# Performance work log

Measured on AMD Instinct MI355X. Metric: run time of the kernel, lower is better.

Reference implementation:

```python
import jax, jax.numpy as jnp
import numpy as np

B, L, H, F, E = 32, 512, 768, 3072, 8  # sentences, seq_len, hidden, ffn, experts


def setup_inputs() -> dict:
    key = jax.random.key(0)
    kx, kl, k1, k2, k3, k4 = jax.random.split(key, 6)
    return {
        "hidden_states": jax.random.normal(kx, (B, L, H), dtype=jnp.float32),
        "router_labels": jax.random.randint(kl, (B,), 0, E, dtype=jnp.int32),
        "W1": jax.random.normal(k1, (E, H, F), dtype=jnp.float32) * 0.02,
        "b1": jnp.zeros((E, F), dtype=jnp.float32),
        "W2": jax.random.normal(k2, (E, F, H), dtype=jnp.float32) * 0.02,
        "b2": jnp.zeros((E, H), dtype=jnp.float32),
    }


def reference(hidden_states, router_labels, W1, b1, W2, b2):
    # Equivalent to: sort sentences by label, run each group through its
    # expert FFN, concat, unsort. Expressed as a gather of per-sentence
    # expert weights followed by batched GEMMs (same math, no data-dependent
    # shapes).
    W1g = W1[router_labels]            # [B, H, F]
    b1g = b1[router_labels][:, None]   # [B, 1, F]
    W2g = W2[router_labels]            # [B, F, H]
    b2g = b2[router_labels][:, None]   # [B, 1, H]
    h = jnp.einsum("blh,bhf->blf", hidden_states, W1g) + b1g
    h = jax.nn.gelu(h, approximate=False)
    out = jnp.einsum("blf,bfh->blh", h, W2g) + b2g
    return out
```

## Files before the change

kernel.cpp:

```cpp
#include <hip/hip_runtime.h>
#include <hip/hip_bf16.h>

#define NB   32
#define SEQ  512
#define HID  768
#define FFN  3072
#define NEXP 8

typedef float f32x4 __attribute__((ext_vector_type(4)));
typedef short s16x8 __attribute__((ext_vector_type(8)));

__device__ __forceinline__ unsigned short f2bf(float f) {
    return __builtin_bit_cast(unsigned short, (__bf16)f);
}

__device__ __forceinline__ float fast_exp2(float x) {
    float r; asm("v_exp_f32 %0, %1" : "=v"(r) : "v"(x)); return r;
}
__device__ __forceinline__ float fast_rcp(float x) {
    float r; asm("v_rcp_f32 %0, %1" : "=v"(r) : "v"(x)); return r;
}

__device__ __forceinline__ float gelu_fast(float v) {
    float u  = v * (0.7978845608f + 0.0356774081f * v * v);
    float t  = fast_exp2(-2.8853900817779268f * fabsf(u));
    float T  = (1.0f - t) * fast_rcp(1.0f + t);
    return 0.5f * v + 0.5f * fabsf(v) * T;
}

#define GLOAD16(gp, lp) __builtin_amdgcn_global_load_lds( \
    (const __attribute__((address_space(1))) unsigned int*)(gp), \
    (__attribute__((address_space(3))) unsigned int*)(lp), 16, 0, 0)

#define VMCNT(N) asm volatile("s_waitcnt vmcnt(%0)" :: "i"(N) : "memory")

__global__ void sort_labels_kernel(const int* __restrict__ labels, int* __restrict__ perm)
{
    int i = threadIdx.x;
    if (i < NB) {
        int li = labels[i];
        int rank = 0;
        for (int j = 0; j < NB; j++) {
            int lj = labels[j];
            if (lj < li || (lj == li && j < i)) rank++;
        }
        perm[rank] = i;
    }
}

__global__ __launch_bounds__(256) void cvt_x_xcd(
    const float* __restrict__ X, const int* __restrict__ perm,
    unsigned short* __restrict__ Xb)
{
    const int L = blockIdx.x;
    const int xcd = L & 7, j = L >> 3;
    const int sent = perm[xcd * 4 + (j >> 3)];
    const int slab = j & 7;
    const size_t base = (size_t)sent * (SEQ * HID) + (size_t)slab * (SEQ * HID / 8);
    const float* src = X + base;
    unsigned short* dst = Xb + base;
    for (int i = threadIdx.x; i < SEQ * HID / 8 / 8; i += 256) {
        f32x4 a = *(const f32x4*)(src + (size_t)i * 8);
        f32x4 b = *(const f32x4*)(src + (size_t)i * 8 + 4);
        unsigned short o[8];
#pragma unroll
        for (int v = 0; v < 4; v++) o[v] = f2bf(a[v]);
#pragma unroll
        for (int v = 0; v < 4; v++) o[4 + v] = f2bf(b[v]);
        *(s16x8*)(dst + (size_t)i * 8) = *(s16x8*)o;
    }
}

__global__ __launch_bounds__(256) void cvt_transpose_kernel(
    const float* __restrict__ W, unsigned short* __restrict__ WT, int R, int C)
{
    __shared__ unsigned short tile[64][65];
    const int cb = blockIdx.x * 64, rb = blockIdx.y * 64;
    const float* src = W + (size_t)blockIdx.z * R * C;
    unsigned short* dst = WT + (size_t)blockIdx.z * R * C;
    const int x = threadIdx.x & 63, y0 = threadIdx.x >> 6;
#pragma unroll
    for (int i = 0; i < 16; i++) {
        int r = y0 + i * 4;
        tile[r][x] = f2bf(src[(size_t)(rb + r) * C + cb + x]);
    }
    __syncthreads();
#pragma unroll
    for (int i = 0; i < 16; i++) {
        int c = y0 + i * 4;
        dst[(size_t)(cb + c) * R + rb + x] = tile[x][c];
    }
}

template<int LDB, bool ISA>
__device__ __forceinline__ void stage_region(const char* g, char* lds, int half, int tid)
{
#pragma unroll
    for (int p = 0; p < 2; p++) {
        int L  = p * 8192 + tid * 16;
        int rr = L >> 7;
        int cb = L & 127;
        int row = ISA ? ((rr & 63) + ((rr >> 6) << 7) + half * 64)
                      : ((rr & 31) + ((rr >> 5) << 6) + half * 32);
        int cbs = cb ^ ((row & 7) << 4);
        GLOAD16(g + (size_t)row * LDB + cbs, lds + (size_t)row * 128 + cb);
    }
}

__device__ __forceinline__ void read_af(const char* Ab, int arow_b, int k0, int ih, s16x8 (&a)[2][4])
{
    const int k1 = k0 ^ 64;
#pragma unroll
    for (int i = 0; i < 4; i++) {
        const char* p = Ab + arow_b + (ih * 64 + i * 16) * 128;
        a[0][i] = *(const s16x8*)(p + k0);
        a[1][i] = *(const s16x8*)(p + k1);
    }
}
__device__ __forceinline__ void read_bf(const char* Bb, int brow_b, int k0, int jh, s16x8 (&b)[2][2])
{
    const int k1 = k0 ^ 64;
#pragma unroll
    for (int j = 0; j < 2; j++) {
        const char* p = Bb + brow_b + (jh * 32 + j * 16) * 128;
        b[0][j] = *(const s16x8*)(p + k0);
        b[1][j] = *(const s16x8*)(p + k1);
    }
}

template<int IH, int JH>
__device__ __forceinline__ void mfma_quad(s16x8 (&a)[2][4], s16x8 (&b)[2][2], f32x4 (&acc)[8][4])
{
    __builtin_amdgcn_s_setprio(1);
#pragma unroll
    for (int kk = 0; kk < 2; kk++)
#pragma unroll
        for (int i = 0; i < 4; i++)
#pragma unroll
            for (int j = 0; j < 2; j++)
                acc[IH * 4 + i][JH * 2 + j] = __builtin_amdgcn_mfma_f32_16x16x32_bf16(
                    a[kk][i], b[kk][j], acc[IH * 4 + i][JH * 2 + j], 0, 0, 0);
    __builtin_amdgcn_s_setprio(0);
}

template<int LDB, bool S1, bool S2, int VM>
__device__ __forceinline__ void gwindow(const char* AgK, const char* BgK,
    char* Acur, char* Bcur, char* Anxt, char* Bnxt,
    int arow_b, int brow_b, int k0, int tid, f32x4 (&acc)[8][4])
{
    s16x8 a[2][4], b0[2][2], b1[2][2];
    read_af(Acur, arow_b, k0, 0, a);
    read_bf(Bcur, brow_b, k0, 0, b0);
    if constexpr (S1) stage_region<LDB, true >(AgK + 128, Anxt, 1, tid);
    __builtin_amdgcn_s_barrier();
    mfma_quad<0, 0>(a, b0, acc);
    __builtin_amdgcn_s_barrier();
    read_bf(Bcur, brow_b, k0, 1, b1);
    if constexpr (S1) stage_region<LDB, false>(BgK + 128, Bnxt, 1, tid);
    __builtin_amdgcn_s_barrier();
    mfma_quad<0, 1>(a, b1, acc);
    __builtin_amdgcn_s_barrier();
    read_af(Acur, arow_b, k0, 1, a);
    if constexpr (S2) stage_region<LDB, true >(AgK + 256, Acur, 0, tid);
    __builtin_amdgcn_s_barrier();
    mfma_quad<1, 1>(a, b1, acc);
    __builtin_amdgcn_s_barrier();
    if constexpr (S2) stage_region<LDB, false>(BgK + 256, Bcur, 0, tid);
    __builtin_amdgcn_s_barrier();
    mfma_quad<1, 0>(a, b0, acc);
    if constexpr (VM >= 0) VMCNT(VM);
    __builtin_amdgcn_s_barrier();
}

template<int LDB>
__device__ __forceinline__ void gemm_mainloop(const char* Ag, const char* Bg,
    char* smem, int KT, int tid, int arow_b, int brow_b, int k0, f32x4 (&acc)[8][4])
{
    stage_region<LDB, true >(Ag,       smem,          0, tid);
    stage_region<LDB, false>(Bg,       smem + 65536,  0, tid);
    stage_region<LDB, true >(Ag,       smem,          1, tid);
    stage_region<LDB, false>(Bg,       smem + 65536,  1, tid);
    stage_region<LDB, true >(Ag + 128, smem + 32768,  0, tid);
    stage_region<LDB, false>(Bg + 128, smem + 98304,  0, tid);
    VMCNT(4);
    __builtin_amdgcn_s_barrier();

    int cur = 0;
    for (int kt = 0; kt < KT - 2; ++kt) {
        char* Acur = smem + (cur << 15);
        char* Anxt = smem + ((cur ^ 1) << 15);
        char* Bcur = smem + 65536 + (cur << 15);
        char* Bnxt = smem + 65536 + ((cur ^ 1) << 15);
        gwindow<LDB, true, true, 4>(Ag + (size_t)kt * 128, Bg + (size_t)kt * 128,
            Acur, Bcur, Anxt, Bnxt, arow_b, brow_b, k0, tid, acc);
        cur ^= 1;
    }
    {
        char* Acur = smem + (cur << 15);
        char* Anxt = smem + ((cur ^ 1) << 15);
        char* Bcur = smem + 65536 + (cur << 15);
        char* Bnxt = smem + 65536 + ((cur ^ 1) << 15);
        gwindow<LDB, true, false, 0>(Ag + (size_t)(KT - 2) * 128, Bg + (size_t)(KT - 2) * 128,
            Acur, Bcur, Anxt, Bnxt, arow_b, brow_b, k0, tid, acc);
        cur ^= 1;
    }
    {
        char* Acur = smem + (cur << 15);
        char* Anxt = smem + ((cur ^ 1) << 15);
        char* Bcur = smem + 65536 + (cur << 15);
        char* Bnxt = smem + 65536 + ((cur ^ 1) << 15);
        gwindow<LDB, false, false, -1>(Ag + (size_t)(KT - 1) * 128, Bg + (size_t)(KT - 1) * 128,
            Acur, Bcur, Anxt, Bnxt, arow_b, brow_b, k0, tid, acc);
    }
}

__global__ __launch_bounds__(512, 2) void moe_gemm1(
    const unsigned short* __restrict__ Xb,
    const int*   __restrict__ labels,
    const int*   __restrict__ perm,
    const unsigned short* __restrict__ W1T,
    const float* __restrict__ B1,
    unsigned short* __restrict__ G)
{
    extern __shared__ char smem[];
    const int L = blockIdx.x;
    const int xcd  = L & 7;
    const int r    = L >> 8;
    const int i    = (L >> 3) & 31;
    const int pair = i >> 2;
    const int bs = perm[xcd * 4 + (pair >> 1)];
    const int mt = pair & 1;
    const int nt = r * 4 + (i & 3);
    const int e  = labels[bs];

    const char* Ag = (const char*)(Xb + ((size_t)bs * SEQ + (size_t)mt * 256) * HID);
    const char* Bg = (const char*)(W1T + (size_t)e * FFN * HID + (size_t)nt * 256 * HID);

    const int tid = threadIdx.x;
    const int lane = tid & 63, w = tid >> 6;
    const int wm = (w >> 2) * 128, wn = (w & 3) * 64;
    const int fr = lane & 15, fq = lane >> 4;
    const int arow_b = (wm + fr) * 128, brow_b = (wn + fr) * 128;
    const int k0 = (fq * 16) ^ ((fr & 7) << 4);

    f32x4 acc[8][4];
#pragma unroll
    for (int i2 = 0; i2 < 8; i2++)
#pragma unroll
        for (int j = 0; j < 4; j++) acc[i2][j] = (f32x4)0.0f;

    gemm_mainloop<HID * 2>(Ag, Bg, smem, HID / 64, tid, arow_b, brow_b, k0, acc);

    const float* b1g = B1 + (size_t)e * FFN + (size_t)nt * 256;
    float bias[4];
#pragma unroll
    for (int nj = 0; nj < 4; nj++) bias[nj] = b1g[wn + nj * 16 + fr];
#pragma unroll
    for (int mi = 0; mi < 8; mi++)
#pragma unroll
        for (int nj = 0; nj < 4; nj++) {
            const int col = wn + nj * 16 + fr;
#pragma unroll
            for (int r2 = 0; r2 < 4; r2++) {
                const int row = wm + mi * 16 + fq * 4 + r2;
                float v = acc[mi][nj][r2] + bias[nj];
                int byte = row * 512 + ((col * 2) ^ ((row & 7) << 4));
                *(unsigned short*)(smem + byte) = f2bf(gelu_fast(v));
            }
        }
    __syncthreads();
    char* Cgb = (char*)(G + ((size_t)bs * SEQ + (size_t)mt * 256) * FFN + (size_t)nt * 256);
#pragma unroll
    for (int it = 0; it < 16; it++) {
        int chunk = tid + it * 512;
        int row = chunk >> 5;
        int cb  = (chunk & 31) * 16;
        s16x8 v = *(const s16x8*)(smem + row * 512 + (cb ^ ((row & 7) << 4)));
        __builtin_nontemporal_store(v, (s16x8*)(Cgb + (size_t)row * (FFN * 2) + cb));
    }
}

__global__ __launch_bounds__(512, 2) void moe_gemm2(
    const unsigned short* __restrict__ G,
    const int*   __restrict__ labels,
    const int*   __restrict__ perm,
    const unsigned short* __restrict__ W2T,
    const float* __restrict__ B2,
    float* __restrict__ Out)
{
    extern __shared__ char smem[];
    const int L = blockIdx.x;
    const int xcd = L & 7, s = L >> 3;
    const int bs = perm[xcd * 4 + s / 6];
    const int rr = s % 6;
    const int mt = rr / 3, nt = rr % 3;
    const int e  = labels[bs];

    const char* Ag = (const char*)(G + ((size_t)bs * SEQ + (size_t)mt * 256) * FFN);
    const char* Bg = (const char*)(W2T + (size_t)e * HID * FFN + (size_t)nt * 256 * FFN);

    const int tid = threadIdx.x;
    const int lane = tid & 63, w = tid >> 6;
    const int wm = (w >> 2) * 128, wn = (w & 3) * 64;
    const int fr = lane & 15, fq = lane >> 4;
    const int arow_b = (wm + fr) * 128, brow_b = (wn + fr) * 128;
    const int k0 = (fq * 16) ^ ((fr & 7) << 4);

    f32x4 acc[8][4];
#pragma unroll
    for (int i = 0; i < 8; i++)
#pragma unroll
        for (int j = 0; j < 4; j++) acc[i][j] = (f32x4)0.0f;

    gemm_mainloop<FFN * 2>(Ag, Bg, smem, FFN / 64, tid, arow_b, brow_b, k0, acc);

    const float* b2g = B2 + (size_t)e * HID + (size_t)nt * 256;
    float bias[4];
#pragma unroll
    for (int nj = 0; nj < 4; nj++) bias[nj] = b2g[wn + nj * 16 + fr];
    char* Cgb = (char*)(Out + ((size_t)bs * SEQ + (size_t)mt * 256) * HID + (size_t)nt * 256);

#pragma unroll
    for (int half = 0; half < 2; ++half) {
        if ((wn >> 7) == half) {
#pragma unroll
            for (int mi = 0; mi < 8; mi++)
#pragma unroll
                for (int nj = 0; nj < 4; nj++) {
                    const int lcol = (wn & 127) + nj * 16 + fr;
#pragma unroll
                    for (int r2 = 0; r2 < 4; r2++) {
                        const int row = wm + mi * 16 + fq * 4 + r2;
                        int byte = row * 512 + ((lcol * 4) ^ ((row & 7) << 4));
                        *(float*)(smem + byte) = acc[mi][nj][r2] + bias[nj];
                    }
                }
        }
        __syncthreads();
#pragma unroll
        for (int it = 0; it < 16; it++) {
            int chunk = tid + it * 512;
            int row = chunk >> 5;
            int cb  = (chunk & 31) * 16;
            f32x4 v = *(const f32x4*)(smem + row * 512 + (cb ^ ((row & 7) << 4)));
            __builtin_nontemporal_store(v, (f32x4*)(Cgb + (size_t)row * (HID * 4) + half * 512 + cb));
        }
        if (half == 0) __syncthreads();
    }
}

extern "C" void kernel_launch(void* const* d_in, const int* in_sizes, int n_in,
                              void* d_out, int out_size, void* d_ws, size_t ws_size,
                              hipStream_t stream) {
    const float* X      = (const float*)d_in[0];
    const int*   labels = (const int*)  d_in[1];
    const float* W1     = (const float*)d_in[2];
    const float* B1     = (const float*)d_in[3];
    const float* W2     = (const float*)d_in[4];
    const float* B2     = (const float*)d_in[5];
    float* Out = (float*)d_out;

    char* ws = (char*)d_ws;
    unsigned short* Xb  = (unsigned short*)(ws);
    unsigned short* W1T = (unsigned short*)(ws + 25165824);
    unsigned short* W2T = (unsigned short*)(ws + 62914560);
    unsigned short* G   = (unsigned short*)(ws + 100663296);
    int*            perm = (int*)(ws + 201326592);

    (void)hipFuncSetAttribute((const void*)moe_gemm1,
        hipFuncAttributeMaxDynamicSharedMemorySize, 131072);
    (void)hipFuncSetAttribute((const void*)moe_gemm2,
        hipFuncAttributeMaxDynamicSharedMemorySize, 131072);

    sort_labels_kernel<<<1, 64, 0, stream>>>(labels, perm);
    cvt_x_xcd<<<256, 256, 0, stream>>>(X, perm, Xb);
    cvt_transpose_kernel<<<dim3(FFN / 64, HID / 64, NEXP), 256, 0, stream>>>(W1, W1T, HID, FFN);
    cvt_transpose_kernel<<<dim3(HID / 64, FFN / 64, NEXP), 256, 0, stream>>>(W2, W2T, FFN, HID);

    moe_gemm1<<<768, dim3(512), 131072, stream>>>(Xb, labels, perm, W1T, B1, G);
    moe_gemm2<<<192, dim3(512), 131072, stream>>>(G, labels, perm, W2T, B2, Out);
}
```

Before: 243.7 us.

## Make GEMM1 blocks loop over three N tiles and simplify X conversion

GEMM1 now launches 256 blocks instead of 768. Each block computes three consecutive 256-wide FFN column tiles in sequence, reusing the same A rows and writing out the bias+GELU results for each tile. The X fp32-to-bf16 conversion becomes a plain grid-stride kernel that no longer orders its work by the sorted-sentence/XCD mapping. With 256 blocks at 2 per CU the grid is a single wave, which avoids tail effects but gives less scheduling slack. The A tile may also lose its warm-L2 placement from the old XCD-ordered conversion.

Measured after the change: 345.2 us. +41.7%, slower.

```diff
diff --git a/kernel.cpp b/kernel.cpp
--- a/kernel.cpp
+++ b/kernel.cpp
@@ -48,26 +48,20 @@
     }
 }
 
-__global__ __launch_bounds__(256) void cvt_x_xcd(
-    const float* __restrict__ X, const int* __restrict__ perm,
-    unsigned short* __restrict__ Xb)
-{
-    const int L = blockIdx.x;
-    const int xcd = L & 7, j = L >> 3;
-    const int sent = perm[xcd * 4 + (j >> 3)];
-    const int slab = j & 7;
-    const size_t base = (size_t)sent * (SEQ * HID) + (size_t)slab * (SEQ * HID / 8);
-    const float* src = X + base;
-    unsigned short* dst = Xb + base;
-    for (int i = threadIdx.x; i < SEQ * HID / 8 / 8; i += 256) {
-        f32x4 a = *(const f32x4*)(src + (size_t)i * 8);
-        f32x4 b = *(const f32x4*)(src + (size_t)i * 8 + 4);
+__global__ __launch_bounds__(256) void cvt_x_kernel(
+    const float* __restrict__ X, unsigned short* __restrict__ Xb, int n8)
+{
+    int idx = blockIdx.x * blockDim.x + threadIdx.x;
+    int stride = gridDim.x * blockDim.x;
+    for (int i = idx; i < n8; i += stride) {
+        f32x4 a = *(const f32x4*)(X + (size_t)i * 8);
+        f32x4 b = *(const f32x4*)(X + (size_t)i * 8 + 4);
         unsigned short o[8];
 #pragma unroll
         for (int v = 0; v < 4; v++) o[v] = f2bf(a[v]);
 #pragma unroll
         for (int v = 0; v < 4; v++) o[4 + v] = f2bf(b[v]);
-        *(s16x8*)(dst + (size_t)i * 8) = *(s16x8*)o;
+        *(s16x8*)(Xb + (size_t)i * 8) = *(s16x8*)o;
     }
 }
 
@@ -225,16 +219,14 @@
     extern __shared__ char smem[];
     const int L = blockIdx.x;
     const int xcd  = L & 7;
-    const int r    = L >> 8;
-    const int i    = (L >> 3) & 31;
-    const int pair = i >> 2;
-    const int bs = perm[xcd * 4 + (pair >> 1)];
-    const int mt = pair & 1;
-    const int nt = r * 4 + (i & 3);
-    const int e  = labels[bs];
+    const int slot = L >> 3;
+    const int pair = slot >> 2;
+    const int bs  = perm[xcd * 4 + (pair >> 1)];
+    const int mt  = pair & 1;
+    const int ntg = slot & 3;
+    const int e   = labels[bs];
 
     const char* Ag = (const char*)(Xb + ((size_t)bs * SEQ + (size_t)mt * 256) * HID);
-    const char* Bg = (const char*)(W1T + (size_t)e * FFN * HID + (size_t)nt * 256 * HID);
 
     const int tid = threadIdx.x;
     const int lane = tid & 63, w = tid >> 6;
@@ -243,40 +235,46 @@
     const int arow_b = (wm + fr) * 128, brow_b = (wn + fr) * 128;
     const int k0 = (fq * 16) ^ ((fr & 7) << 4);
 
-    f32x4 acc[8][4];
-#pragma unroll
-    for (int i2 = 0; i2 < 8; i2++)
-#pragma unroll
-        for (int j = 0; j < 4; j++) acc[i2][j] = (f32x4)0.0f;
-
-    gemm_mainloop<HID * 2>(Ag, Bg, smem, HID / 64, tid, arow_b, brow_b, k0, acc);
-
-    const float* b1g = B1 + (size_t)e * FFN + (size_t)nt * 256;
-    float bias[4];
-#pragma unroll
-    for (int nj = 0; nj < 4; nj++) bias[nj] = b1g[wn + nj * 16 + fr];
-#pragma unroll
-    for (int mi = 0; mi < 8; mi++)
-#pragma unroll
-        for (int nj = 0; nj < 4; nj++) {
-            const int col = wn + nj * 16 + fr;
-#pragma unroll
-            for (int r2 = 0; r2 < 4; r2++) {
-                const int row = wm + mi * 16 + fq * 4 + r2;
-                float v = acc[mi][nj][r2] + bias[nj];
-                int byte = row * 512 + ((col * 2) ^ ((row & 7) << 4));
-                *(unsigned short*)(smem + byte) = f2bf(gelu_fast(v));
+    for (int chunk = 0; chunk < 3; ++chunk) {
+        const int nt = ntg * 3 + chunk;
+        const char* Bg = (const char*)(W1T + (size_t)e * FFN * HID + (size_t)nt * 256 * HID);
+
+        f32x4 acc[8][4];
+#pragma unroll
+        for (int i2 = 0; i2 < 8; i2++)
+#pragma unroll
+            for (int j = 0; j < 4; j++) acc[i2][j] = (f32x4)0.0f;
+
+        gemm_mainloop<HID * 2>(Ag, Bg, smem, HID / 64, tid, arow_b, brow_b, k0, acc);
+
+        const float* b1g = B1 + (size_t)e * FFN + (size_t)nt * 256;
+        float bias[4];
+#pragma unroll
+        for (int nj = 0; nj < 4; nj++) bias[nj] = b1g[wn + nj * 16 + fr];
+#pragma unroll
+        for (int mi = 0; mi < 8; mi++)
+#pragma unroll
+            for (int nj = 0; nj < 4; nj++) {
+                const int col = wn + nj * 16 + fr;
+#pragma unroll
+                for (int r2 = 0; r2 < 4; r2++) {
+                    const int row = wm + mi * 16 + fq * 4 + r2;
+                    float v = acc[mi][nj][r2] + bias[nj];
+                    int byte = row * 512 + ((col * 2) ^ ((row & 7) << 4));
+                    *(unsigned short*)(smem + byte) = f2bf(gelu_fast(v));
+                }
             }
+        __syncthreads();
+        char* Cgb = (char*)(G + ((size_t)bs * SEQ + (size_t)mt * 256) * FFN + (size_t)nt * 256);
+#pragma unroll
+        for (int it = 0; it < 16; it++) {
+            int c2 = tid + it * 512;
+            int row = c2 >> 5;
+            int cb  = (c2 & 31) * 16;
+            s16x8 v = *(const s16x8*)(smem + row * 512 + (cb ^ ((row & 7) << 4)));
+            __builtin_nontemporal_store(v, (s16x8*)(Cgb + (size_t)row * (FFN * 2) + cb));
         }
-    __syncthreads();
-    char* Cgb = (char*)(G + ((size_t)bs * SEQ + (size_t)mt * 256) * FFN + (size_t)nt * 256);
-#pragma unroll
-    for (int it = 0; it < 16; it++) {
-        int chunk = tid + it * 512;
-        int row = chunk >> 5;
-        int cb  = (chunk & 31) * 16;
-        s16x8 v = *(const s16x8*)(smem + row * 512 + (cb ^ ((row & 7) << 4)));
-        __builtin_nontemporal_store(v, (s16x8*)(Cgb + (size_t)row * (FFN * 2) + cb));
+        __syncthreads();
     }
 }
 
@@ -373,10 +371,10 @@
         hipFuncAttributeMaxDynamicSharedMemorySize, 131072);
 
     sort_labels_kernel<<<1, 64, 0, stream>>>(labels, perm);
-    cvt_x_xcd<<<256, 256, 0, stream>>>(X, perm, Xb);
+    cvt_x_kernel<<<2048, 256, 0, stream>>>(X, Xb, NB * SEQ * HID / 8);
     cvt_transpose_kernel<<<dim3(FFN / 64, HID / 64, NEXP), 256, 0, stream>>>(W1, W1T, HID, FFN);
     cvt_transpose_kernel<<<dim3(HID / 64, FFN / 64, NEXP), 256, 0, stream>>>(W2, W2T, FFN, HID);
 
-    moe_gemm1<<<768, dim3(512), 131072, stream>>>(Xb, labels, perm, W1T, B1, G);
+    moe_gemm1<<<256, dim3(512), 131072, stream>>>(Xb, labels, perm, W1T, B1, G);
     moe_gemm2<<<192, dim3(512), 131072, stream>>>(G, labels, perm, W2T, B2, Out);
 }
```

## Pre-pack operands into contiguous swizzled 32KB tiles for linear LDS staging

Applied to the files above, without the earlier changes.

Changes the conversion kernels so X, W1, W2 and the intermediate G are written in a tile-packed layout. Each 256x64 K-slab becomes a contiguous 32KB block with the LDS XOR swizzle already applied. The GEMM main loops then issue fully linear global-to-LDS loads instead of strided row loads, which aims to improve DRAM/L2 access locality. The cost is more complex index math in the pack kernels and the GEMM1 epilogue. The X conversion also no longer uses the perm-based XCD ordering.

New measurement: 239.1 us. About the same (-1.9%).

```diff
diff --git a/kernel.cpp b/kernel.cpp
--- a/kernel.cpp
+++ b/kernel.cpp
@@ -33,6 +33,7 @@
     (__attribute__((address_space(3))) unsigned int*)(lp), 16, 0, 0)
 
 #define VMCNT(N) asm volatile("s_waitcnt vmcnt(%0)" :: "i"(N) : "memory")
+
 
 __global__ void sort_labels_kernel(const int* __restrict__ labels, int* __restrict__ perm)
 {
@@ -48,52 +49,78 @@
     }
 }
 
-__global__ __launch_bounds__(256) void cvt_x_xcd(
-    const float* __restrict__ X, const int* __restrict__ perm,
-    unsigned short* __restrict__ Xb)
-{
-    const int L = blockIdx.x;
-    const int xcd = L & 7, j = L >> 3;
-    const int sent = perm[xcd * 4 + (j >> 3)];
-    const int slab = j & 7;
-    const size_t base = (size_t)sent * (SEQ * HID) + (size_t)slab * (SEQ * HID / 8);
-    const float* src = X + base;
-    unsigned short* dst = Xb + base;
-    for (int i = threadIdx.x; i < SEQ * HID / 8 / 8; i += 256) {
-        f32x4 a = *(const f32x4*)(src + (size_t)i * 8);
-        f32x4 b = *(const f32x4*)(src + (size_t)i * 8 + 4);
+__global__ __launch_bounds__(256) void cvt_x_pack(
+    const float* __restrict__ X, unsigned short* __restrict__ XbP)
+{
+    const int b  = blockIdx.x;
+    const int kt = b % 12;
+    const int mt = (b / 12) & 1;
+    const int bs = b / 24;
+    const float* src = X + ((size_t)bs * SEQ + (size_t)mt * 256) * HID + kt * 64;
+    char* out = (char*)XbP + (size_t)b * 32768;
+
+#pragma unroll
+    for (int i = 0; i < 8; i++) {
+        int c = threadIdx.x + i * 256;
+        int half = c >> 10;
+        int rr   = (c >> 3) & 127;
+        int c16  = c & 7;
+        int row  = (rr & 63) + ((rr >> 6) << 7) + half * 64;
+        int tb   = (c16 * 16) ^ ((row & 7) << 4);
+        int k0e  = tb >> 1;
+        const float* sp = src + (size_t)row * HID + k0e;
+        f32x4 a = *(const f32x4*)sp;
+        f32x4 b4 = *(const f32x4*)(sp + 4);
         unsigned short o[8];
 #pragma unroll
         for (int v = 0; v < 4; v++) o[v] = f2bf(a[v]);
 #pragma unroll
-        for (int v = 0; v < 4; v++) o[4 + v] = f2bf(b[v]);
-        *(s16x8*)(dst + (size_t)i * 8) = *(s16x8*)o;
-    }
-}
-
-__global__ __launch_bounds__(256) void cvt_transpose_kernel(
-    const float* __restrict__ W, unsigned short* __restrict__ WT, int R, int C)
+        for (int v = 0; v < 4; v++) o[4 + v] = f2bf(b4[v]);
+        *(s16x8*)(out + (size_t)c * 16) = *(s16x8*)o;
+    }
+}
+
+__global__ __launch_bounds__(256) void cvt_w_pack(
+    const float* __restrict__ W, unsigned short* __restrict__ WP)
 {
     __shared__ unsigned short tile[64][65];
-    const int cb = blockIdx.x * 64, rb = blockIdx.y * 64;
-    const float* src = W + (size_t)blockIdx.z * R * C;
-    unsigned short* dst = WT + (size_t)blockIdx.z * R * C;
+    const int e   = blockIdx.z;
+    const int C   = gridDim.x * 64;
+    const int R   = gridDim.y * 64;
+    const int cbg = blockIdx.x * 64;
+    const int rbg = blockIdx.y * 64;
+    const float* src = W + (size_t)e * R * C;
     const int x = threadIdx.x & 63, y0 = threadIdx.x >> 6;
 #pragma unroll
     for (int i = 0; i < 16; i++) {
         int r = y0 + i * 4;
-        tile[r][x] = f2bf(src[(size_t)(rb + r) * C + cb + x]);
+        tile[r][x] = f2bf(src[(size_t)(rbg + r) * C + cbg + x]);
     }
     __syncthreads();
-#pragma unroll
-    for (int i = 0; i < 16; i++) {
-        int c = y0 + i * 4;
-        dst[(size_t)(cb + c) * R + rb + x] = tile[x][c];
-    }
-}
-
-template<int LDB, bool ISA>
-__device__ __forceinline__ void stage_region(const char* g, char* lds, int half, int tid)
+
+    const int nt  = blockIdx.x >> 2;
+    const int NTn = gridDim.x >> 2;
+    const int kt  = blockIdx.y;
+    const int KT  = gridDim.y;
+    char* out = (char*)WP + ((size_t)(e * NTn + nt) * KT + kt) * 32768;
+
+#pragma unroll
+    for (int i = 0; i < 2; i++) {
+        int cc  = threadIdx.x + i * 256;
+        int n64 = cc >> 3, kc = cc & 7;
+        int row = (blockIdx.x & 3) * 64 + n64;
+        int half = (row >> 5) & 1;
+        int rr   = (row & 31) | (((row >> 6) & 3) << 5);
+        int q    = (kc * 16) ^ ((row & 7) << 4);
+        unsigned short o[8];
+#pragma unroll
+        for (int j = 0; j < 8; j++) o[j] = tile[kc * 8 + j][n64];
+        *(s16x8*)(out + half * 16384 + rr * 128 + q) = *(s16x8*)o;
+    }
+}
+
+template<bool ISA>
+__device__ __forceinline__ void stage_lin(const char* tile, char* lds, int half, int tid)
 {
 #pragma unroll
     for (int p = 0; p < 2; p++) {
@@ -102,8 +129,7 @@
         int cb = L & 127;
         int row = ISA ? ((rr & 63) + ((rr >> 6) << 7) + half * 64)
                       : ((rr & 31) + ((rr >> 5) << 6) + half * 32);
-        int cbs = cb ^ ((row & 7) << 4);
-        GLOAD16(g + (size_t)row * LDB + cbs, lds + (size_t)row * 128 + cb);
+        GLOAD16(tile + half * 16384 + L, lds + (size_t)row * 128 + cb);
     }
 }
 
@@ -143,84 +169,85 @@
     __builtin_amdgcn_s_setprio(0);
 }
 
-template<int LDB, bool S1, bool S2, int VM>
-__device__ __forceinline__ void gwindow(const char* AgK, const char* BgK,
+template<bool S1, bool S2, int VM>
+__device__ __forceinline__ void gwindowT(
+    const char* tA1, const char* tB1, const char* tA0, const char* tB0,
     char* Acur, char* Bcur, char* Anxt, char* Bnxt,
     int arow_b, int brow_b, int k0, int tid, f32x4 (&acc)[8][4])
 {
     s16x8 a[2][4], b0[2][2], b1[2][2];
     read_af(Acur, arow_b, k0, 0, a);
     read_bf(Bcur, brow_b, k0, 0, b0);
-    if constexpr (S1) stage_region<LDB, true >(AgK + 128, Anxt, 1, tid);
+    if constexpr (S1) stage_lin<true >(tA1, Anxt, 1, tid);
     __builtin_amdgcn_s_barrier();
     mfma_quad<0, 0>(a, b0, acc);
     __builtin_amdgcn_s_barrier();
     read_bf(Bcur, brow_b, k0, 1, b1);
-    if constexpr (S1) stage_region<LDB, false>(BgK + 128, Bnxt, 1, tid);
+    if constexpr (S1) stage_lin<false>(tB1, Bnxt, 1, tid);
     __builtin_amdgcn_s_barrier();
     mfma_quad<0, 1>(a, b1, acc);
     __builtin_amdgcn_s_barrier();
     read_af(Acur, arow_b, k0, 1, a);
-    if constexpr (S2) stage_region<LDB, true >(AgK + 256, Acur, 0, tid);
+    if constexpr (S2) stage_lin<true >(tA0, Acur, 0, tid);
     __builtin_amdgcn_s_barrier();
     mfma_quad<1, 1>(a, b1, acc);
     __builtin_amdgcn_s_barrier();
-    if constexpr (S2) stage_region<LDB, false>(BgK + 256, Bcur, 0, tid);
+    if constexpr (S2) stage_lin<false>(tB0, Bcur, 0, tid);
     __builtin_amdgcn_s_barrier();
     mfma_quad<1, 0>(a, b0, acc);
     if constexpr (VM >= 0) VMCNT(VM);
     __builtin_amdgcn_s_barrier();
 }
 
-template<int LDB>
-__device__ __forceinline__ void gemm_mainloop(const char* Ag, const char* Bg,
-    char* smem, int KT, int tid, int arow_b, int brow_b, int k0, f32x4 (&acc)[8][4])
-{
-    stage_region<LDB, true >(Ag,       smem,          0, tid);
-    stage_region<LDB, false>(Bg,       smem + 65536,  0, tid);
-    stage_region<LDB, true >(Ag,       smem,          1, tid);
-    stage_region<LDB, false>(Bg,       smem + 65536,  1, tid);
-    stage_region<LDB, true >(Ag + 128, smem + 32768,  0, tid);
-    stage_region<LDB, false>(Bg + 128, smem + 98304,  0, tid);
+__device__ __forceinline__ void mainloopT(const char* At, const char* Bt, int KT,
+    char* smem, int tid, int arow_b, int brow_b, int k0, f32x4 (&acc)[8][4])
+{
+    stage_lin<true >(At,          smem,          0, tid);
+    stage_lin<false>(Bt,          smem + 65536,  0, tid);
+    stage_lin<true >(At,          smem,          1, tid);
+    stage_lin<false>(Bt,          smem + 65536,  1, tid);
+    stage_lin<true >(At + 32768,  smem + 32768,  0, tid);
+    stage_lin<false>(Bt + 32768,  smem + 98304,  0, tid);
     VMCNT(4);
     __builtin_amdgcn_s_barrier();
 
     int cur = 0;
     for (int kt = 0; kt < KT - 2; ++kt) {
-        char* Acur = smem + (cur << 15);
-        char* Anxt = smem + ((cur ^ 1) << 15);
-        char* Bcur = smem + 65536 + (cur << 15);
-        char* Bnxt = smem + 65536 + ((cur ^ 1) << 15);
-        gwindow<LDB, true, true, 4>(Ag + (size_t)kt * 128, Bg + (size_t)kt * 128,
-            Acur, Bcur, Anxt, Bnxt, arow_b, brow_b, k0, tid, acc);
+        char* Ac = smem + (cur << 15);
+        char* An = smem + ((cur ^ 1) << 15);
+        char* Bc = smem + 65536 + (cur << 15);
+        char* Bn = smem + 65536 + ((cur ^ 1) << 15);
+        gwindowT<true, true, 4>(At + (size_t)(kt + 1) * 32768, Bt + (size_t)(kt + 1) * 32768,
+                                At + (size_t)(kt + 2) * 32768, Bt + (size_t)(kt + 2) * 32768,
+                                Ac, Bc, An, Bn, arow_b, brow_b, k0, tid, acc);
         cur ^= 1;
     }
     {
-        char* Acur = smem + (cur << 15);
-        char* Anxt = smem + ((cur ^ 1) << 15);
-        char* Bcur = smem + 65536 + (cur << 15);
-        char* Bnxt = smem + 65536 + ((cur ^ 1) << 15);
-        gwindow<LDB, true, false, 0>(Ag + (size_t)(KT - 2) * 128, Bg + (size_t)(KT - 2) * 128,
-            Acur, Bcur, Anxt, Bnxt, arow_b, brow_b, k0, tid, acc);
+        char* Ac = smem + (cur << 15);
+        char* An = smem + ((cur ^ 1) << 15);
+        char* Bc = smem + 65536 + (cur << 15);
+        char* Bn = smem + 65536 + ((cur ^ 1) << 15);
+        gwindowT<true, false, 0>(At + (size_t)(KT - 1) * 32768, Bt + (size_t)(KT - 1) * 32768,
+                                 nullptr, nullptr, Ac, Bc, An, Bn, arow_b, brow_b, k0, tid, acc);
         cur ^= 1;
     }
     {
-        char* Acur = smem + (cur << 15);
-        char* Anxt = smem + ((cur ^ 1) << 15);
-        char* Bcur = smem + 65536 + (cur << 15);
-        char* Bnxt = smem + 65536 + ((cur ^ 1) << 15);
-        gwindow<LDB, false, false, -1>(Ag + (size_t)(KT - 1) * 128, Bg + (size_t)(KT - 1) * 128,
-            Acur, Bcur, Anxt, Bnxt, arow_b, brow_b, k0, tid, acc);
+        char* Ac = smem + (cur << 15);
+        char* An = smem + ((cur ^ 1) << 15);
+        char* Bc = smem + 65536 + (cur << 15);
+        char* Bn = smem + 65536 + ((cur ^ 1) << 15);
+        gwindowT<false, false, -1>(nullptr, nullptr, nullptr, nullptr,
+                                   Ac, Bc, An, Bn, arow_b, brow_b, k0, tid, acc);
     }
 }
 
 __global__ __launch_bounds__(512, 2) void moe_gemm1(
-    const unsigned short* __restrict__ Xb,
+    const unsigned short* __restrict__ XbP,
     const int*   __restrict__ labels,
     const int*   __restrict__ perm,
-    const unsigned short* __restrict__ W1T,
+    const unsigned short* __restrict__ W1P,
     const float* __restrict__ B1,
-    unsigned short* __restrict__ G)
+    unsigned short* __restrict__ GP)
 {
     extern __shared__ char smem[];
     const int L = blockIdx.x;
@@ -233,8 +260,8 @@
     const int nt = r * 4 + (i & 3);
     const int e  = labels[bs];
 
-    const char* Ag = (const char*)(Xb + ((size_t)bs * SEQ + (size_t)mt * 256) * HID);
-    const char* Bg = (const char*)(W1T + (size_t)e * FFN * HID + (size_t)nt * 256 * HID);
+    const char* At = (const char*)XbP + (size_t)((bs * 2 + mt) * 12) * 32768;
+    const char* Bt = (const char*)W1P + (size_t)((e * 12 + nt) * 12) * 32768;
 
     const int tid = threadIdx.x;
     const int lane = tid & 63, w = tid >> 6;
@@ -249,7 +276,7 @@
 #pragma unroll
         for (int j = 0; j < 4; j++) acc[i2][j] = (f32x4)0.0f;
 
-    gemm_mainloop<HID * 2>(Ag, Bg, smem, HID / 64, tid, arow_b, brow_b, k0, acc);
+    mainloopT(At, Bt, 12, smem, tid, arow_b, brow_b, k0, acc);
 
     const float* b1g = B1 + (size_t)e * FFN + (size_t)nt * 256;
     float bias[4];
@@ -269,22 +296,26 @@
             }
         }
     __syncthreads();
-    char* Cgb = (char*)(G + ((size_t)bs * SEQ + (size_t)mt * 256) * FFN + (size_t)nt * 256);
+    char* GPb = (char*)GP + ((size_t)(bs * 2 + mt) * 48 + (size_t)nt * 4) * 32768;
 #pragma unroll
     for (int it = 0; it < 16; it++) {
-        int chunk = tid + it * 512;
-        int row = chunk >> 5;
-        int cb  = (chunk & 31) * 16;
-        s16x8 v = *(const s16x8*)(smem + row * 512 + (cb ^ ((row & 7) << 4)));
-        __builtin_nontemporal_store(v, (s16x8*)(Cgb + (size_t)row * (FFN * 2) + cb));
+        int c2 = tid + it * 512;
+        int kt2l = c2 >> 11;
+        int reg  = (c2 >> 10) & 1;
+        int rr2  = (c2 >> 3) & 127;
+        int c16  = c2 & 7;
+        int row  = (rr2 & 63) + ((rr2 >> 6) << 7) + reg * 64;
+        s16x8 v = *(const s16x8*)(smem + row * 512 + kt2l * 128 + c16 * 16);
+        __builtin_nontemporal_store(v,
+            (s16x8*)(GPb + (size_t)kt2l * 32768 + (size_t)(c2 & 2047) * 16));
     }
 }
 
 __global__ __launch_bounds__(512, 2) void moe_gemm2(
-    const unsigned short* __restrict__ G,
+    const unsigned short* __restrict__ GP,
     const int*   __restrict__ labels,
     const int*   __restrict__ perm,
-    const unsigned short* __restrict__ W2T,
+    const unsigned short* __restrict__ W2P,
     const float* __restrict__ B2,
     float* __restrict__ Out)
 {
@@ -296,8 +327,8 @@
     const int mt = rr / 3, nt = rr % 3;
     const int e  = labels[bs];
 
-    const char* Ag = (const char*)(G + ((size_t)bs * SEQ + (size_t)mt * 256) * FFN);
-    const char* Bg = (const char*)(W2T + (size_t)e * HID * FFN + (size_t)nt * 256 * FFN);
+    const char* At = (const char*)GP  + (size_t)((bs * 2 + mt) * 48) * 32768;
+    const char* Bt = (const char*)W2P + (size_t)((e * 3 + nt) * 48) * 32768;
 
     const int tid = threadIdx.x;
     const int lane = tid & 63, w = tid >> 6;
@@ -312,7 +343,7 @@
 #pragma unroll
         for (int j = 0; j < 4; j++) acc[i][j] = (f32x4)0.0f;
 
-    gemm_mainloop<FFN * 2>(Ag, Bg, smem, FFN / 64, tid, arow_b, brow_b, k0, acc);
+    mainloopT(At, Bt, 48, smem, tid, arow_b, brow_b, k0, acc);
 
     const float* b2g = B2 + (size_t)e * HID + (size_t)nt * 256;
     float bias[4];
@@ -361,10 +392,10 @@
     float* Out = (float*)d_out;
 
     char* ws = (char*)d_ws;
-    unsigned short* Xb  = (unsigned short*)(ws);
-    unsigned short* W1T = (unsigned short*)(ws + 25165824);
-    unsigned short* W2T = (unsigned short*)(ws + 62914560);
-    unsigned short* G   = (unsigned short*)(ws + 100663296);
+    unsigned short* XbP = (unsigned short*)(ws);
+    unsigned short* W1P = (unsigned short*)(ws + 25165824);
+    unsigned short* W2P = (unsigned short*)(ws + 62914560);
+    unsigned short* GP  = (unsigned short*)(ws + 100663296);
     int*            perm = (int*)(ws + 201326592);
 
     (void)hipFuncSetAttribute((const void*)moe_gemm1,
@@ -373,10 +404,10 @@
         hipFuncAttributeMaxDynamicSharedMemorySize, 131072);
 
     sort_labels_kernel<<<1, 64, 0, stream>>>(labels, perm);
-    cvt_x_xcd<<<256, 256, 0, stream>>>(X, perm, Xb);
-    cvt_transpose_kernel<<<dim3(FFN / 64, HID / 64, NEXP), 256, 0, stream>>>(W1, W1T, HID, FFN);
-    cvt_transpose_kernel<<<dim3(HID / 64, FFN / 64, NEXP), 256, 0, stream>>>(W2, W2T, FFN, HID);
-
-    moe_gemm1<<<768, dim3(512), 131072, stream>>>(Xb, labels, perm, W1T, B1, G);
-    moe_gemm2<<<192, dim3(512), 131072, stream>>>(G, labels, perm, W2T, B2, Out);
-}
+    cvt_x_pack<<<768, 256, 0, stream>>>(X, XbP);
+    cvt_w_pack<<<dim3(FFN / 64, HID / 64, NEXP), 256, 0, stream>>>(W1, W1P);
+    cvt_w_pack<<<dim3(HID / 64, FFN / 64, NEXP), 256, 0, stream>>>(W2, W2P);
+
+    moe_gemm1<<<768, dim3(512), 131072, stream>>>(XbP, labels, perm, W1P, B1, GP);
+    moe_gemm2<<<192, dim3(512), 131072, stream>>>(GP, labels, perm, W2P, B2, Out);
+}
```
